# Kernel optimization log

Measured on AMD Instinct MI355X. Metric: run time of the kernel, lower is better.

## Reference

```python
import jax, jax.numpy as jnp
import numpy as np


def setup_inputs() -> dict:
    key = jax.random.key(0)
    k1, k2, k3 = jax.random.split(key, 3)
    B, D, N, C = 4096, 256, 65536, 10
    x = jax.random.normal(k1, (B, D), dtype=jnp.float32)
    keys = jax.random.normal(k2, (N, D), dtype=jnp.float32)
    values = jax.random.uniform(k3, (N, C), dtype=jnp.float32)
    return {"x": x, "keys": keys, "values": values, "k": 8}


def reference(x, keys, values, k):
    # squared euclidean distances [B, N] without materializing diff cube:
    x_sq = jnp.sum(x * x, axis=1, keepdims=True)          # [B,1]
    k_sq = jnp.sum(keys * keys, axis=1)                   # [N]
    dists = x_sq - 2.0 * (x @ keys.T) + k_sq[None, :]     # [B,N]
    neg_top, indices = jax.lax.top_k(-dists, k)           # [B,k]
    hit_values = values[indices]                          # [B,k,C]
    return jnp.sum(hit_values, axis=1) / jnp.float32(k)   # [B,C]
```

## Files before the change

### kernel.cpp

```cpp
#include <hip/hip_runtime.h>
#include <stdint.h>
#include <float.h>

#define B_ROWS 4096
#define N_KEYS 65536
#define DDIM 256
#define NCH 10

#define NSPLIT 8
#define SPLIT_KEYS (N_KEYS / NSPLIT)
#define ROWS_PER_BLK 64
#define CHUNK_KEYS 64
#define NCHUNK (SPLIT_KEYS / CHUNK_KEYS)

typedef float f32x4 __attribute__((ext_vector_type(4)));
typedef short bf16x8 __attribute__((ext_vector_type(8)));

static __device__ __forceinline__ unsigned short f2bf(float f) {
  unsigned u = __float_as_uint(f);
  return (unsigned short)((u + 0x7FFFu + ((u >> 16) & 1u)) >> 16);
}
static __device__ __forceinline__ unsigned ford(float f) {
  unsigned u = __float_as_uint(f);
  return u ^ ((unsigned)((int)u >> 31) | 0x80000000u);
}
static __device__ __forceinline__ unsigned long long shfl_xor_u64(unsigned long long v, int m) {
  unsigned lo = __shfl_xor((unsigned)v, m, 64);
  unsigned hi = __shfl_xor((unsigned)(v >> 32), m, 64);
  return ((unsigned long long)hi << 32) | lo;
}
static __device__ __forceinline__ double shfl_xor_f64(double v, int m) {
  return __longlong_as_double((long long)shfl_xor_u64((unsigned long long)__double_as_longlong(v), m));
}
static __device__ __forceinline__ void gl_lds16(const void* g, void* l) {
  __builtin_amdgcn_global_load_lds(
      (const __attribute__((address_space(1))) unsigned int*)g,
      (__attribute__((address_space(3))) unsigned int*)l, 16, 0, 0);
}

__global__ __launch_bounds__(256) void transpose_keys(const float* __restrict__ keys,
                                                      unsigned char* __restrict__ kbf,
                                                      float* __restrict__ ksq) {
  __shared__ __align__(16) unsigned char T[128 * 512];
  const int t = threadIdx.x;
  const int lane = t & 63;
  const float4* src = (const float4*)(keys + (size_t)blockIdx.x * 128 * DDIM);
#pragma unroll
  for (int j = 0; j < 32; ++j) {
    int g = j * 256 + t;
    float4 v = src[g];
    int key = g >> 6;
    int u = lane >> 1, sub = lane & 1;
    unsigned lo = ((unsigned)f2bf(v.y) << 16) | f2bf(v.x);
    unsigned hi2 = ((unsigned)f2bf(v.w) << 16) | f2bf(v.z);
    unsigned long long p = ((unsigned long long)hi2 << 32) | lo;
    *(unsigned long long*)&T[key * 512 + ((u ^ (key & 7)) << 4) + (sub << 3)] = p;
    float ss = v.x * v.x + v.y * v.y + v.z * v.z + v.w * v.w;
#pragma unroll
    for (int off = 32; off; off >>= 1) ss += __shfl_xor(ss, off, 64);
    if (lane == 0) ksq[blockIdx.x * 128 + key] = ss;
  }
  __syncthreads();
  uint4* dst = (uint4*)(kbf + (size_t)blockIdx.x * 65536);
#pragma unroll
  for (int j = 0; j < 16; ++j) {
    int ou = j * 256 + t;
    int c64 = ou >> 11, rem = ou & 2047;
    int koct = rem >> 6, key64 = rem & 63;
    int keyl = c64 * 64 + key64;
    dst[ou] = *(const uint4*)&T[keyl * 512 + ((koct ^ (keyl & 7)) << 4)];
  }
}

__global__ __launch_bounds__(512, 4) void knn_main(
    const float* __restrict__ x,
    const unsigned char* __restrict__ kbf,
    const float* __restrict__ ksqg,
    unsigned int* __restrict__ pools,
    unsigned int* __restrict__ counts,
    int CAP) {
  __shared__ __align__(16) unsigned char tiles[2][32768];
  __shared__ float tauh[2][2][2][16][4];
  __shared__ unsigned int rowcnt[64];

  const int t = threadIdx.x;
  const int lane = t & 63;
  const int wv = t >> 6;
  const int mw = wv & 3;
  const int ws = wv >> 2;
  const int lo4 = lane & 15;
  const int hi = lane >> 4;

  const int split = blockIdx.x & (NSPLIT - 1);
  const int rb = (blockIdx.x >> 3) * ROWS_PER_BLK;
  const int sb = split * SPLIT_KEYS;

  const int xrow0 = rb + ws * 32 + lo4;
  const int xrow1 = xrow0 + 16;
  const int rl0 = ws * 32 + lo4, rl1 = rl0 + 16;

  bf16x8 xb0[8], xb1[8];
#pragma unroll
  for (int s = 0; s < 8; ++s) {
    const float* p0 = x + (size_t)xrow0 * DDIM + s * 32 + hi * 8;
    const float* p1 = x + (size_t)xrow1 * DDIM + s * 32 + hi * 8;
    float4 a = *(const float4*)p0, b = *(const float4*)(p0 + 4);
    float4 c = *(const float4*)p1, d = *(const float4*)(p1 + 4);
    union { unsigned short us[8]; bf16x8 v; } u0, u1;
    u0.us[0]=f2bf(a.x); u0.us[1]=f2bf(a.y); u0.us[2]=f2bf(a.z); u0.us[3]=f2bf(a.w);
    u0.us[4]=f2bf(b.x); u0.us[5]=f2bf(b.y); u0.us[6]=f2bf(b.z); u0.us[7]=f2bf(b.w);
    u1.us[0]=f2bf(c.x); u1.us[1]=f2bf(c.y); u1.us[2]=f2bf(c.z); u1.us[3]=f2bf(c.w);
    u1.us[4]=f2bf(d.x); u1.us[5]=f2bf(d.y); u1.us[6]=f2bf(d.z); u1.us[7]=f2bf(d.w);
    xb0[s] = u0.v; xb1[s] = u1.v;
  }

  float smin0 = FLT_MAX, smin1 = FLT_MAX;
  const unsigned char* srcbase = kbf + ((size_t)split * NCHUNK << 15);
  const size_t pb0 = ((size_t)xrow0 * NSPLIT + split) * (size_t)CAP;
  const size_t pb1 = ((size_t)xrow1 * NSPLIT + split) * (size_t)CAP;

  auto STAGE = [&](int c, int buf) {
    const unsigned char* src = srcbase + ((size_t)c << 15);
    unsigned char* wb = (unsigned char*)tiles[buf] + ((wv * 64) << 4);
#pragma unroll
    for (int i = 0; i < 4; ++i)
      gl_lds16(src + (((i * 512) + t) << 4), wb + ((i * 512) << 4));
  };

  f32x4 a0, a1;
  float sc0[4], sc1[4];

  auto COMPUTE = [&](int c) {
    const unsigned char* tile = tiles[c & 1];
    a0 = 0.0f; a1 = 0.0f;
#pragma unroll
    for (int s = 0; s < 8; ++s) {
      const unsigned char* rp = tile + (s * 4 + hi) * 1024 + (mw * 16 + lo4) * 16;
      bf16x8 af = *(const bf16x8*)rp;
      a0 = __builtin_amdgcn_mfma_f32_16x16x32_bf16(af, xb0[s], a0, 0, 0, 0);
      a1 = __builtin_amdgcn_mfma_f32_16x16x32_bf16(af, xb1[s], a1, 0, 0, 0);
    }
    float4 kq = *(const float4*)(ksqg + sb + c * CHUNK_KEYS + mw * 16 + hi * 4);
#pragma unroll
    for (int i = 0; i < 4; ++i) {
      sc0[i] = fmaf(-2.0f, a0[i], ((const float*)&kq)[i]);
      sc1[i] = fmaf(-2.0f, a1[i], ((const float*)&kq)[i]);
    }
    float mb0 = fminf(fminf(sc0[0], sc0[1]), fminf(sc0[2], sc0[3]));
    float mb1 = fminf(fminf(sc1[0], sc1[1]), fminf(sc1[2], sc1[3]));
    smin0 = fminf(smin0, mb0);
    smin1 = fminf(smin1, mb1);
  };

  auto PUBLISH = [&](int par) {
    float p0 = fminf(smin0, __shfl_xor(smin0, 16, 64));
    p0 = fmaxf(p0, __shfl_xor(p0, 32, 64));
    float p1 = fminf(smin1, __shfl_xor(smin1, 16, 64));
    p1 = fmaxf(p1, __shfl_xor(p1, 32, 64));
    if (hi == 0) {
      tauh[par][0][ws][lo4][mw] = p0;
      tauh[par][1][ws][lo4][mw] = p1;
    }
  };

  auto APPEND = [&](int c, int par) {
    float4 t0 = *(const float4*)&tauh[par][0][ws][lo4][0];
    float4 t1 = *(const float4*)&tauh[par][1][ws][lo4][0];
    float tau0 = fmaxf(fmaxf(t0.x, t0.y), fmaxf(t0.z, t0.w));
    float tau1 = fmaxf(fmaxf(t1.x, t1.y), fmaxf(t1.z, t1.w));
    int kloc = c * CHUNK_KEYS + mw * 16 + hi * 4;
#pragma unroll
    for (int e = 0; e < 4; ++e) {
      if (sc0[e] <= tau0) {
        unsigned slot = atomicAdd(&rowcnt[rl0], 1u);
        if ((int)slot < CAP)
          pools[pb0 + slot] = (ford(sc0[e]) & 0xFFFFE000u) | (unsigned)(kloc + e);
      }
      if (sc1[e] <= tau1) {
        unsigned slot = atomicAdd(&rowcnt[rl1], 1u);
        if ((int)slot < CAP)
          pools[pb1 + slot] = (ford(sc1[e]) & 0xFFFFE000u) | (unsigned)(kloc + e);
      }
    }
  };

  if (t < 64) rowcnt[t] = 0;
  STAGE(0, 0);
  __syncthreads();
  STAGE(1, 1);
  COMPUTE(0);
  PUBLISH(0);
  PUBLISH(1);
  __syncthreads();
  APPEND(0, 0);

#pragma unroll 1
  for (int c = 1; c < NCHUNK; ++c) {
    const int cn = (c + 1 < NCHUNK) ? c + 1 : c;
    STAGE(cn, (c + 1) & 1);
    COMPUTE(c);
    APPEND(c, (c - 1) & 1);
    PUBLISH(c & 1);
    __syncthreads();
  }

  __syncthreads();
  if (t < 64) counts[(size_t)(rb + t) * NSPLIT + split] = rowcnt[t];
}

__global__ __launch_bounds__(64) void knn_refine(
    const float* __restrict__ x,
    const float* __restrict__ keys,
    const float* __restrict__ ksq,
    const float* __restrict__ values,
    const unsigned int* __restrict__ pools,
    const unsigned int* __restrict__ counts,
    int CAP,
    float* __restrict__ out) {
  __shared__ float4 xl[64];
  const int row = blockIdx.x;
  const int lane = threadIdx.x;

  xl[lane] = ((const float4*)(x + (size_t)row * DDIM))[lane];
  __syncthreads();

  unsigned long long h[8];
#pragma unroll
  for (int i = 0; i < 8; ++i) h[i] = ~0ULL;

  auto insert = [&](unsigned long long v) {
    if (v < h[7]) {
#pragma unroll
      for (int j = 7; j >= 1; --j) {
        unsigned long long a = h[j - 1];
        unsigned long long mx = a > v ? a : v;
        h[j] = (v < h[j]) ? mx : h[j];
      }
      h[0] = h[0] < v ? h[0] : v;
    }
  };

  for (int s = 0; s < NSPLIT; ++s) {
    unsigned cnt = counts[(size_t)row * NSPLIT + s];
    if ((int)cnt <= CAP) {
      const unsigned int* pp = pools + ((size_t)row * NSPLIT + s) * (size_t)CAP;
      for (int i = lane; i < (int)cnt; i += 64) {
        unsigned p = pp[i];
        unsigned long long v = ((unsigned long long)p << 17)
                             | (unsigned)(s * SPLIT_KEYS + (p & 0x1FFFu));
        insert(v);
      }
    } else {
      for (int kk = lane; kk < SPLIT_KEYS; kk += 64) {
        int gk = s * SPLIT_KEYS + kk;
        const float4* kr = (const float4*)(keys + (size_t)gk * DDIM);
        float acc = 0.f;
#pragma unroll 8
        for (int d = 0; d < 64; ++d) {
          float4 kv = kr[d], xv = xl[d];
          acc = fmaf(kv.x, xv.x, acc); acc = fmaf(kv.y, xv.y, acc);
          acc = fmaf(kv.z, xv.z, acc); acc = fmaf(kv.w, xv.w, acc);
        }
        float sc = fmaf(-2.0f, acc, ksq[gk]);
        unsigned p = (ford(sc) & 0xFFFFE000u) | (unsigned)kk;
        insert(((unsigned long long)p << 17) | (unsigned)gk);
      }
    }
  }

  int myidx = 0;
#pragma unroll 1
  for (int r = 0; r < 24; ++r) {
    unsigned long long m = h[0];
#pragma unroll
    for (int off = 32; off; off >>= 1) {
      unsigned long long o = shfl_xor_u64(m, off);
      m = o < m ? o : m;
    }
    if (lane == r) myidx = (int)(m & 0x1FFFFu);
    if (h[0] == m) {
#pragma unroll
      for (int i = 0; i < 7; ++i) h[i] = h[i + 1];
      h[7] = ~0ULL;
    }
  }

  double dv = 1e300;
  if (lane < 24) {
    const float4* kr = (const float4*)(keys + (size_t)myidx * DDIM);
    double s = 0.0;
#pragma unroll 8
    for (int d = 0; d < 64; ++d) {
      float4 kv = kr[d], xv = xl[d];
      double d0 = (double)xv.x - (double)kv.x;
      double d1 = (double)xv.y - (double)kv.y;
      double d2 = (double)xv.z - (double)kv.z;
      double d3 = (double)xv.w - (double)kv.w;
      s += d0 * d0 + d1 * d1 + d2 * d2 + d3 * d3;
    }
    dv = s;
  }

  int di = myidx;
  int chosen[8];
#pragma unroll
  for (int r = 0; r < 8; ++r) {
    double m = dv; int mi = di;
#pragma unroll
    for (int off = 32; off; off >>= 1) {
      double om = shfl_xor_f64(m, off);
      int omi = __shfl_xor(mi, off, 64);
      if (om < m || (om == m && omi < mi)) { m = om; mi = omi; }
    }
    chosen[r] = mi;
    if (di == mi && dv < 1e300) dv = 1e300;
  }

  if (lane < NCH) {
    double a = 0.0;
#pragma unroll
    for (int r = 0; r < 8; ++r) a += (double)values[(size_t)chosen[r] * NCH + lane];
    out[row * NCH + lane] = (float)(a * 0.125);
  }
}

extern "C" void kernel_launch(void* const* d_in, const int* in_sizes, int n_in,
                              void* d_out, int out_size, void* d_ws, size_t ws_size,
                              hipStream_t stream) {
  (void)in_sizes; (void)n_in; (void)out_size;
  const float* x      = (const float*)d_in[0];
  const float* keys   = (const float*)d_in[1];
  const float* values = (const float*)d_in[2];
  float* out = (float*)d_out;

  char* ws = (char*)d_ws;
  unsigned char* kbf = (unsigned char*)ws;
  float* ksq   = (float*)(ws + 33554432);
  unsigned int* counts = (unsigned int*)(ws + 33554432 + 262144);
  unsigned int* pools  = (unsigned int*)(ws + 33554432 + 262144 + 131072);

  size_t base = 33554432 + 262144 + 131072;
  size_t cap = (ws_size > base) ? (ws_size - base) / ((size_t)B_ROWS * NSPLIT * 4) : 32;
  if (cap < 32) cap = 32;
  if (cap > 2048) cap = 2048;
  int CAP = (int)cap;

  transpose_keys<<<N_KEYS / 128, 256, 0, stream>>>(keys, kbf, ksq);
  knn_main<<<(B_ROWS / ROWS_PER_BLK) * NSPLIT, 512, 0, stream>>>(
      x, kbf, ksq, pools, counts, CAP);
  knn_refine<<<B_ROWS, 64, 0, stream>>>(x, keys, ksq, values, pools, counts, CAP, out);
}
```

Baseline: 318.6 us.

## Enlarge row tile per block to reuse staged key tiles across more MFMAs

Each block now processes 256 query rows against a 1/16 key split instead of 64 rows against a 1/8 split. Each wave holds four 16-row x fragments and two key fragments, so every LDS key load feeds more MFMAs and global key traffic per row drops. The threshold selection is reworked so each chunk is filtered against the previous chunk's published per-row thresholds. The loop synchronisation uses explicit waitcnt and barriers with ksq prefetch. Pool index encoding shrinks to 12 bits. Register pressure rises (launch bounds drop to 2 blocks per SIMD) and the grid shrinks to 256 blocks, which may reduce occupancy.

```diff
diff --git a/kernel.cpp b/kernel.cpp
--- a/kernel.cpp
+++ b/kernel.cpp
@@ -7,9 +7,9 @@
 #define DDIM 256
 #define NCH 10
 
-#define NSPLIT 8
+#define NSPLIT 16
 #define SPLIT_KEYS (N_KEYS / NSPLIT)
-#define ROWS_PER_BLK 64
+#define ROWS_PER_BLK 256
 #define CHUNK_KEYS 64
 #define NCHUNK (SPLIT_KEYS / CHUNK_KEYS)
 
@@ -72,7 +72,7 @@
   }
 }
 
-__global__ __launch_bounds__(512, 4) void knn_main(
+__global__ __launch_bounds__(512, 2) void knn_main(
     const float* __restrict__ x,
     const unsigned char* __restrict__ kbf,
     const float* __restrict__ ksqg,
@@ -80,44 +80,39 @@
     unsigned int* __restrict__ counts,
     int CAP) {
   __shared__ __align__(16) unsigned char tiles[2][32768];
-  __shared__ float tauh[2][2][2][16][4];
-  __shared__ unsigned int rowcnt[64];
+  __shared__ float tauh[2][256];
+  __shared__ unsigned int rowcnt[256];
 
   const int t = threadIdx.x;
   const int lane = t & 63;
   const int wv = t >> 6;
-  const int mw = wv & 3;
-  const int ws = wv >> 2;
+  const int kg = wv & 1;
+  const int rq = wv >> 1;
   const int lo4 = lane & 15;
   const int hi = lane >> 4;
 
   const int split = blockIdx.x & (NSPLIT - 1);
-  const int rb = (blockIdx.x >> 3) * ROWS_PER_BLK;
+  const int rb = (blockIdx.x >> 4) * ROWS_PER_BLK;
   const int sb = split * SPLIT_KEYS;
 
-  const int xrow0 = rb + ws * 32 + lo4;
-  const int xrow1 = xrow0 + 16;
-  const int rl0 = ws * 32 + lo4, rl1 = rl0 + 16;
-
-  bf16x8 xb0[8], xb1[8];
-#pragma unroll
-  for (int s = 0; s < 8; ++s) {
-    const float* p0 = x + (size_t)xrow0 * DDIM + s * 32 + hi * 8;
-    const float* p1 = x + (size_t)xrow1 * DDIM + s * 32 + hi * 8;
-    float4 a = *(const float4*)p0, b = *(const float4*)(p0 + 4);
-    float4 c = *(const float4*)p1, d = *(const float4*)(p1 + 4);
-    union { unsigned short us[8]; bf16x8 v; } u0, u1;
-    u0.us[0]=f2bf(a.x); u0.us[1]=f2bf(a.y); u0.us[2]=f2bf(a.z); u0.us[3]=f2bf(a.w);
-    u0.us[4]=f2bf(b.x); u0.us[5]=f2bf(b.y); u0.us[6]=f2bf(b.z); u0.us[7]=f2bf(b.w);
-    u1.us[0]=f2bf(c.x); u1.us[1]=f2bf(c.y); u1.us[2]=f2bf(c.z); u1.us[3]=f2bf(c.w);
-    u1.us[4]=f2bf(d.x); u1.us[5]=f2bf(d.y); u1.us[6]=f2bf(d.z); u1.us[7]=f2bf(d.w);
-    xb0[s] = u0.v; xb1[s] = u1.v;
-  }
-
-  float smin0 = FLT_MAX, smin1 = FLT_MAX;
-  const unsigned char* srcbase = kbf + ((size_t)split * NCHUNK << 15);
-  const size_t pb0 = ((size_t)xrow0 * NSPLIT + split) * (size_t)CAP;
-  const size_t pb1 = ((size_t)xrow1 * NSPLIT + split) * (size_t)CAP;
+  bf16x8 xb[4][8];
+#pragma unroll
+  for (int st = 0; st < 4; ++st) {
+    const float* xr = x + (size_t)(rb + rq * 64 + st * 16 + lo4) * DDIM;
+#pragma unroll
+    for (int s = 0; s < 8; ++s) {
+      const float* p = xr + s * 32 + hi * 8;
+      float4 a = *(const float4*)p, b = *(const float4*)(p + 4);
+      union { unsigned short us[8]; bf16x8 v; } u;
+      u.us[0]=f2bf(a.x); u.us[1]=f2bf(a.y); u.us[2]=f2bf(a.z); u.us[3]=f2bf(a.w);
+      u.us[4]=f2bf(b.x); u.us[5]=f2bf(b.y); u.us[6]=f2bf(b.z); u.us[7]=f2bf(b.w);
+      xb[st][s] = u.v;
+    }
+  }
+
+  if (t < 256) rowcnt[t] = 0;
+
+  const unsigned char* srcbase = kbf + ((size_t)(split * NCHUNK) << 15);
 
   auto STAGE = [&](int c, int buf) {
     const unsigned char* src = srcbase + ((size_t)c << 15);
@@ -127,85 +122,119 @@
       gl_lds16(src + (((i * 512) + t) << 4), wb + ((i * 512) << 4));
   };
 
-  f32x4 a0, a1;
-  float sc0[4], sc1[4];
+  const int kqoff = kg * 32 + hi * 4;
+  float4 kqc0 = *(const float4*)(ksqg + sb + kqoff);
+  float4 kqc1 = *(const float4*)(ksqg + sb + kqoff + 16);
+
+  float smin[4] = {FLT_MAX, FLT_MAX, FLT_MAX, FLT_MAX};
+  f32x4 acc[4][2];
 
   auto COMPUTE = [&](int c) {
     const unsigned char* tile = tiles[c & 1];
-    a0 = 0.0f; a1 = 0.0f;
+#pragma unroll
+    for (int st = 0; st < 4; ++st) { acc[st][0] = 0.0f; acc[st][1] = 0.0f; }
 #pragma unroll
     for (int s = 0; s < 8; ++s) {
-      const unsigned char* rp = tile + (s * 4 + hi) * 1024 + (mw * 16 + lo4) * 16;
-      bf16x8 af = *(const bf16x8*)rp;
-      a0 = __builtin_amdgcn_mfma_f32_16x16x32_bf16(af, xb0[s], a0, 0, 0, 0);
-      a1 = __builtin_amdgcn_mfma_f32_16x16x32_bf16(af, xb1[s], a1, 0, 0, 0);
-    }
-    float4 kq = *(const float4*)(ksqg + sb + c * CHUNK_KEYS + mw * 16 + hi * 4);
-#pragma unroll
-    for (int i = 0; i < 4; ++i) {
-      sc0[i] = fmaf(-2.0f, a0[i], ((const float*)&kq)[i]);
-      sc1[i] = fmaf(-2.0f, a1[i], ((const float*)&kq)[i]);
-    }
-    float mb0 = fminf(fminf(sc0[0], sc0[1]), fminf(sc0[2], sc0[3]));
-    float mb1 = fminf(fminf(sc1[0], sc1[1]), fminf(sc1[2], sc1[3]));
-    smin0 = fminf(smin0, mb0);
-    smin1 = fminf(smin1, mb1);
-  };
-
-  auto PUBLISH = [&](int par) {
-    float p0 = fminf(smin0, __shfl_xor(smin0, 16, 64));
-    p0 = fmaxf(p0, __shfl_xor(p0, 32, 64));
-    float p1 = fminf(smin1, __shfl_xor(smin1, 16, 64));
-    p1 = fmaxf(p1, __shfl_xor(p1, 32, 64));
-    if (hi == 0) {
-      tauh[par][0][ws][lo4][mw] = p0;
-      tauh[par][1][ws][lo4][mw] = p1;
-    }
-  };
-
-  auto APPEND = [&](int c, int par) {
-    float4 t0 = *(const float4*)&tauh[par][0][ws][lo4][0];
-    float4 t1 = *(const float4*)&tauh[par][1][ws][lo4][0];
-    float tau0 = fmaxf(fmaxf(t0.x, t0.y), fmaxf(t0.z, t0.w));
-    float tau1 = fmaxf(fmaxf(t1.x, t1.y), fmaxf(t1.z, t1.w));
-    int kloc = c * CHUNK_KEYS + mw * 16 + hi * 4;
-#pragma unroll
-    for (int e = 0; e < 4; ++e) {
-      if (sc0[e] <= tau0) {
-        unsigned slot = atomicAdd(&rowcnt[rl0], 1u);
-        if ((int)slot < CAP)
-          pools[pb0 + slot] = (ford(sc0[e]) & 0xFFFFE000u) | (unsigned)(kloc + e);
-      }
-      if (sc1[e] <= tau1) {
-        unsigned slot = atomicAdd(&rowcnt[rl1], 1u);
-        if ((int)slot < CAP)
-          pools[pb1 + slot] = (ford(sc1[e]) & 0xFFFFE000u) | (unsigned)(kloc + e);
-      }
-    }
-  };
-
-  if (t < 64) rowcnt[t] = 0;
+      const unsigned char* rp = tile + (s * 4 + hi) * 1024 + (kg * 32 + lo4) * 16;
+      bf16x8 af0 = *(const bf16x8*)rp;
+      bf16x8 af1 = *(const bf16x8*)(rp + 256);
+#pragma unroll
+      for (int st = 0; st < 4; ++st) {
+        acc[st][0] = __builtin_amdgcn_mfma_f32_16x16x32_bf16(af0, xb[st][s], acc[st][0], 0, 0, 0);
+        acc[st][1] = __builtin_amdgcn_mfma_f32_16x16x32_bf16(af1, xb[st][s], acc[st][1], 0, 0, 0);
+      }
+    }
+  };
+
+  auto SELECT = [&](int c, const float* trd) {
+    const int kbase = c * CHUNK_KEYS + kg * 32;
+#pragma unroll
+    for (int st = 0; st < 4; ++st) {
+      float sc[8];
+#pragma unroll
+      for (int i = 0; i < 4; ++i) {
+        sc[i]     = fmaf(-2.0f, acc[st][0][i], ((const float*)&kqc0)[i]);
+        sc[4 + i] = fmaf(-2.0f, acc[st][1][i], ((const float*)&kqc1)[i]);
+      }
+      float m = sc[0];
+#pragma unroll
+      for (int e = 1; e < 8; ++e) m = fminf(m, sc[e]);
+      smin[st] = fminf(smin[st], m);
+      if (m <= trd[st]) {
+        const int lrow = rq * 64 + st * 16 + lo4;
+        const size_t pb = ((size_t)(rb + lrow) * NSPLIT + split) * (size_t)CAP;
+#pragma unroll
+        for (int e = 0; e < 8; ++e) {
+          if (sc[e] <= trd[st]) {
+            unsigned slot = atomicAdd(&rowcnt[lrow], 1u);
+            if ((int)slot < CAP)
+              pools[pb + slot] = (ford(sc[e]) & 0xFFFFF000u)
+                               | (unsigned)(kbase + (e >> 2) * 16 + hi * 4 + (e & 3));
+          }
+        }
+      }
+    }
+  };
+
+  auto PUBLISH = [&]() {
+#pragma unroll
+    for (int st = 0; st < 4; ++st) {
+      float v = smin[st];
+      v = fmaxf(v, __shfl_xor(v, 16, 64));
+      v = fmaxf(v, __shfl_xor(v, 32, 64));
+      if (hi == 0) tauh[kg][rq * 64 + st * 16 + lo4] = v;
+    }
+  };
+
   STAGE(0, 0);
   __syncthreads();
+
   STAGE(1, 1);
+  float4 kqn0 = *(const float4*)(ksqg + sb + 64 + kqoff);
+  float4 kqn1 = *(const float4*)(ksqg + sb + 64 + kqoff + 16);
   COMPUTE(0);
-  PUBLISH(0);
-  PUBLISH(1);
-  __syncthreads();
-  APPEND(0, 0);
+  {
+    float tneg[4] = {-FLT_MAX, -FLT_MAX, -FLT_MAX, -FLT_MAX};
+    SELECT(0, tneg);
+  }
+  PUBLISH();
+  __syncthreads();
+  {
+    float trd[4];
+#pragma unroll
+    for (int st = 0; st < 4; ++st) {
+      int lr = rq * 64 + st * 16 + lo4;
+      trd[st] = fmaxf(tauh[0][lr], tauh[1][lr]);
+    }
+    SELECT(0, trd);
+  }
+  kqc0 = kqn0; kqc1 = kqn1;
 
 #pragma unroll 1
   for (int c = 1; c < NCHUNK; ++c) {
     const int cn = (c + 1 < NCHUNK) ? c + 1 : c;
     STAGE(cn, (c + 1) & 1);
+    float4 kn0 = *(const float4*)(ksqg + sb + cn * 64 + kqoff);
+    float4 kn1 = *(const float4*)(ksqg + sb + cn * 64 + kqoff + 16);
+    float trd[4];
+#pragma unroll
+    for (int st = 0; st < 4; ++st) {
+      int lr = rq * 64 + st * 16 + lo4;
+      trd[st] = fmaxf(tauh[0][lr], tauh[1][lr]);
+    }
+    asm volatile("s_waitcnt vmcnt(6)" ::: "memory");
+    __builtin_amdgcn_s_barrier();
+    __builtin_amdgcn_sched_barrier(0);
     COMPUTE(c);
-    APPEND(c, (c - 1) & 1);
-    PUBLISH(c & 1);
-    __syncthreads();
-  }
-
-  __syncthreads();
-  if (t < 64) counts[(size_t)(rb + t) * NSPLIT + split] = rowcnt[t];
+    SELECT(c, trd);
+    PUBLISH();
+    kqc0 = kn0; kqc1 = kn1;
+    asm volatile("s_waitcnt lgkmcnt(0)" ::: "memory");
+    __builtin_amdgcn_s_barrier();
+  }
+
+  __syncthreads();
+  if (t < 256) counts[(size_t)(rb + t) * NSPLIT + split] = rowcnt[t];
 }
 
 __global__ __launch_bounds__(64) void knn_refine(
@@ -246,8 +275,8 @@
       const unsigned int* pp = pools + ((size_t)row * NSPLIT + s) * (size_t)CAP;
       for (int i = lane; i < (int)cnt; i += 64) {
         unsigned p = pp[i];
-        unsigned long long v = ((unsigned long long)p << 17)
-                             | (unsigned)(s * SPLIT_KEYS + (p & 0x1FFFu));
+        unsigned long long v = ((unsigned long long)p << 16)
+                             | (unsigned)(s * SPLIT_KEYS + (p & 0xFFFu));
         insert(v);
       }
     } else {
@@ -262,8 +291,8 @@
           acc = fmaf(kv.z, xv.z, acc); acc = fmaf(kv.w, xv.w, acc);
         }
         float sc = fmaf(-2.0f, acc, ksq[gk]);
-        unsigned p = (ford(sc) & 0xFFFFE000u) | (unsigned)kk;
-        insert(((unsigned long long)p << 17) | (unsigned)gk);
+        unsigned p = (ford(sc) & 0xFFFFF000u) | (unsigned)kk;
+        insert(((unsigned long long)p << 16) | (unsigned)gk);
       }
     }
   }
@@ -277,7 +306,7 @@
       unsigned long long o = shfl_xor_u64(m, off);
       m = o < m ? o : m;
     }
-    if (lane == r) myidx = (int)(m & 0x1FFFFu);
+    if (lane == r) myidx = (int)(m & 0xFFFFu);
     if (h[0] == m) {
 #pragma unroll
       for (int i = 0; i < 7; ++i) h[i] = h[i + 1];
@@ -337,12 +366,12 @@
   unsigned char* kbf = (unsigned char*)ws;
   float* ksq   = (float*)(ws + 33554432);
   unsigned int* counts = (unsigned int*)(ws + 33554432 + 262144);
-  unsigned int* pools  = (unsigned int*)(ws + 33554432 + 262144 + 131072);
-
-  size_t base = 33554432 + 262144 + 131072;
+  unsigned int* pools  = (unsigned int*)(ws + 33554432 + 262144 + 262144);
+
+  size_t base = 33554432 + 262144 + 262144;
   size_t cap = (ws_size > base) ? (ws_size - base) / ((size_t)B_ROWS * NSPLIT * 4) : 32;
   if (cap < 32) cap = 32;
-  if (cap > 2048) cap = 2048;
+  if (cap > 1024) cap = 1024;
   int CAP = (int)cap;
 
   transpose_keys<<<N_KEYS / 128, 256, 0, stream>>>(keys, kbf, ksq);
```

Result: slower. 341.8 us (+7.3%).

## Restructure kNN main kernel to register-streamed keys with global shared thresholds

Applied to the files above, without the earlier changes.

Replaces the LDS-staged key tiles with direct global-to-register loads of a new key layout. Each wave now holds 64 query rows in registers and streams 16-key slices, with double-buffered prefetch. Splits grow from 8 to 32, and candidates go into one per-row pool through global atomics. A global per-row threshold (atomicMin) is shared across splits to prune appends, and a separate kernel pre-converts x to bf16. The goal is to remove LDS traffic and block-level syncs and to raise MFMA reuse of each key fragment. The cost is more global atomics, heavier register pressure, and some dependence on cross-block threshold timing.

```diff
diff --git a/kernel.cpp b/kernel.cpp
--- a/kernel.cpp
+++ b/kernel.cpp
@@ -7,11 +7,9 @@
 #define DDIM 256
 #define NCH 10
 
-#define NSPLIT 8
+#define NSPLIT 32
 #define SPLIT_KEYS (N_KEYS / NSPLIT)
-#define ROWS_PER_BLK 64
-#define CHUNK_KEYS 64
-#define NCHUNK (SPLIT_KEYS / CHUNK_KEYS)
+#define NSTEP (SPLIT_KEYS / 16)
 
 typedef float f32x4 __attribute__((ext_vector_type(4)));
 typedef short bf16x8 __attribute__((ext_vector_type(8)));
@@ -23,6 +21,10 @@
 static __device__ __forceinline__ unsigned ford(float f) {
   unsigned u = __float_as_uint(f);
   return u ^ ((unsigned)((int)u >> 31) | 0x80000000u);
+}
+static __device__ __forceinline__ float ford_inv(unsigned u) {
+  unsigned m = 0x80000000u | ((u >> 31) - 1u);
+  return __uint_as_float(u ^ m);
 }
 static __device__ __forceinline__ unsigned long long shfl_xor_u64(unsigned long long v, int m) {
   unsigned lo = __shfl_xor((unsigned)v, m, 64);
@@ -31,11 +33,6 @@
 }
 static __device__ __forceinline__ double shfl_xor_f64(double v, int m) {
   return __longlong_as_double((long long)shfl_xor_u64((unsigned long long)__double_as_longlong(v), m));
-}
-static __device__ __forceinline__ void gl_lds16(const void* g, void* l) {
-  __builtin_amdgcn_global_load_lds(
-      (const __attribute__((address_space(1))) unsigned int*)g,
-      (__attribute__((address_space(3))) unsigned int*)l, 16, 0, 0);
 }
 
 __global__ __launch_bounds__(256) void transpose_keys(const float* __restrict__ keys,
@@ -61,151 +58,157 @@
     if (lane == 0) ksq[blockIdx.x * 128 + key] = ss;
   }
   __syncthreads();
-  uint4* dst = (uint4*)(kbf + (size_t)blockIdx.x * 65536);
+  uint4* dstS = (uint4*)(kbf + (size_t)(blockIdx.x >> 4) * ((size_t)SPLIT_KEYS * 512));
+  const int kb0 = (blockIdx.x & 15) * 128;
 #pragma unroll
   for (int j = 0; j < 16; ++j) {
     int ou = j * 256 + t;
-    int c64 = ou >> 11, rem = ou & 2047;
-    int koct = rem >> 6, key64 = rem & 63;
-    int keyl = c64 * 64 + key64;
-    dst[ou] = *(const uint4*)&T[keyl * 512 + ((koct ^ (keyl & 7)) << 4)];
-  }
-}
-
-__global__ __launch_bounds__(512, 4) void knn_main(
-    const float* __restrict__ x,
+    int koct = ou >> 7, keyl = ou & 127;
+    dstS[koct * SPLIT_KEYS + kb0 + keyl] =
+        *(const uint4*)&T[keyl * 512 + ((koct ^ (keyl & 7)) << 4)];
+  }
+}
+
+__global__ __launch_bounds__(256) void xprep(const float* __restrict__ x,
+                                             unsigned char* __restrict__ xbf,
+                                             unsigned int* __restrict__ counts,
+                                             unsigned int* __restrict__ taug) {
+  int u = blockIdx.x * 256 + threadIdx.x;
+  int g = u >> 9, s = (u >> 6) & 7, lane = u & 63;
+  int row = g * 16 + (lane & 15);
+  int d0 = s * 32 + (lane >> 4) * 8;
+  const float* p = x + (size_t)row * DDIM + d0;
+  float4 a = *(const float4*)p, b = *(const float4*)(p + 4);
+  union { unsigned short us[8]; bf16x8 v; } w;
+  w.us[0]=f2bf(a.x); w.us[1]=f2bf(a.y); w.us[2]=f2bf(a.z); w.us[3]=f2bf(a.w);
+  w.us[4]=f2bf(b.x); w.us[5]=f2bf(b.y); w.us[6]=f2bf(b.z); w.us[7]=f2bf(b.w);
+  *(bf16x8*)(xbf + (size_t)u * 16) = w.v;
+  if (u < B_ROWS) { counts[u] = 0; taug[u] = 0xFF7FFFFFu; }
+}
+
+__global__ __launch_bounds__(256, 2) void knn_main(
+    const unsigned char* __restrict__ xbf,
     const unsigned char* __restrict__ kbf,
     const float* __restrict__ ksqg,
-    unsigned int* __restrict__ pools,
+    unsigned long long* __restrict__ pool,
     unsigned int* __restrict__ counts,
+    unsigned int* __restrict__ taug,
     int CAP) {
-  __shared__ __align__(16) unsigned char tiles[2][32768];
-  __shared__ float tauh[2][2][2][16][4];
-  __shared__ unsigned int rowcnt[64];
-
   const int t = threadIdx.x;
   const int lane = t & 63;
   const int wv = t >> 6;
-  const int mw = wv & 3;
-  const int ws = wv >> 2;
   const int lo4 = lane & 15;
   const int hi = lane >> 4;
 
   const int split = blockIdx.x & (NSPLIT - 1);
-  const int rb = (blockIdx.x >> 3) * ROWS_PER_BLK;
+  const int rb = (blockIdx.x >> 5) * 256 + wv * 64;
   const int sb = split * SPLIT_KEYS;
 
-  const int xrow0 = rb + ws * 32 + lo4;
-  const int xrow1 = xrow0 + 16;
-  const int rl0 = ws * 32 + lo4, rl1 = rl0 + 16;
-
-  bf16x8 xb0[8], xb1[8];
-#pragma unroll
-  for (int s = 0; s < 8; ++s) {
-    const float* p0 = x + (size_t)xrow0 * DDIM + s * 32 + hi * 8;
-    const float* p1 = x + (size_t)xrow1 * DDIM + s * 32 + hi * 8;
-    float4 a = *(const float4*)p0, b = *(const float4*)(p0 + 4);
-    float4 c = *(const float4*)p1, d = *(const float4*)(p1 + 4);
-    union { unsigned short us[8]; bf16x8 v; } u0, u1;
-    u0.us[0]=f2bf(a.x); u0.us[1]=f2bf(a.y); u0.us[2]=f2bf(a.z); u0.us[3]=f2bf(a.w);
-    u0.us[4]=f2bf(b.x); u0.us[5]=f2bf(b.y); u0.us[6]=f2bf(b.z); u0.us[7]=f2bf(b.w);
-    u1.us[0]=f2bf(c.x); u1.us[1]=f2bf(c.y); u1.us[2]=f2bf(c.z); u1.us[3]=f2bf(c.w);
-    u1.us[4]=f2bf(d.x); u1.us[5]=f2bf(d.y); u1.us[6]=f2bf(d.z); u1.us[7]=f2bf(d.w);
-    xb0[s] = u0.v; xb1[s] = u1.v;
-  }
-
-  float smin0 = FLT_MAX, smin1 = FLT_MAX;
-  const unsigned char* srcbase = kbf + ((size_t)split * NCHUNK << 15);
-  const size_t pb0 = ((size_t)xrow0 * NSPLIT + split) * (size_t)CAP;
-  const size_t pb1 = ((size_t)xrow1 * NSPLIT + split) * (size_t)CAP;
-
-  auto STAGE = [&](int c, int buf) {
-    const unsigned char* src = srcbase + ((size_t)c << 15);
-    unsigned char* wb = (unsigned char*)tiles[buf] + ((wv * 64) << 4);
-#pragma unroll
-    for (int i = 0; i < 4; ++i)
-      gl_lds16(src + (((i * 512) + t) << 4), wb + ((i * 512) << 4));
-  };
-
-  f32x4 a0, a1;
-  float sc0[4], sc1[4];
-
-  auto COMPUTE = [&](int c) {
-    const unsigned char* tile = tiles[c & 1];
-    a0 = 0.0f; a1 = 0.0f;
-#pragma unroll
-    for (int s = 0; s < 8; ++s) {
-      const unsigned char* rp = tile + (s * 4 + hi) * 1024 + (mw * 16 + lo4) * 16;
-      bf16x8 af = *(const bf16x8*)rp;
-      a0 = __builtin_amdgcn_mfma_f32_16x16x32_bf16(af, xb0[s], a0, 0, 0, 0);
-      a1 = __builtin_amdgcn_mfma_f32_16x16x32_bf16(af, xb1[s], a1, 0, 0, 0);
-    }
-    float4 kq = *(const float4*)(ksqg + sb + c * CHUNK_KEYS + mw * 16 + hi * 4);
-#pragma unroll
-    for (int i = 0; i < 4; ++i) {
-      sc0[i] = fmaf(-2.0f, a0[i], ((const float*)&kq)[i]);
-      sc1[i] = fmaf(-2.0f, a1[i], ((const float*)&kq)[i]);
-    }
-    float mb0 = fminf(fminf(sc0[0], sc0[1]), fminf(sc0[2], sc0[3]));
-    float mb1 = fminf(fminf(sc1[0], sc1[1]), fminf(sc1[2], sc1[3]));
-    smin0 = fminf(smin0, mb0);
-    smin1 = fminf(smin1, mb1);
-  };
-
-  auto PUBLISH = [&](int par) {
-    float p0 = fminf(smin0, __shfl_xor(smin0, 16, 64));
-    p0 = fmaxf(p0, __shfl_xor(p0, 32, 64));
-    float p1 = fminf(smin1, __shfl_xor(smin1, 16, 64));
-    p1 = fmaxf(p1, __shfl_xor(p1, 32, 64));
-    if (hi == 0) {
-      tauh[par][0][ws][lo4][mw] = p0;
-      tauh[par][1][ws][lo4][mw] = p1;
-    }
-  };
-
-  auto APPEND = [&](int c, int par) {
-    float4 t0 = *(const float4*)&tauh[par][0][ws][lo4][0];
-    float4 t1 = *(const float4*)&tauh[par][1][ws][lo4][0];
-    float tau0 = fmaxf(fmaxf(t0.x, t0.y), fmaxf(t0.z, t0.w));
-    float tau1 = fmaxf(fmaxf(t1.x, t1.y), fmaxf(t1.z, t1.w));
-    int kloc = c * CHUNK_KEYS + mw * 16 + hi * 4;
-#pragma unroll
-    for (int e = 0; e < 4; ++e) {
-      if (sc0[e] <= tau0) {
-        unsigned slot = atomicAdd(&rowcnt[rl0], 1u);
-        if ((int)slot < CAP)
-          pools[pb0 + slot] = (ford(sc0[e]) & 0xFFFFE000u) | (unsigned)(kloc + e);
+  bf16x8 xb[4][8];
+#pragma unroll
+  for (int st = 0; st < 4; ++st)
+#pragma unroll
+    for (int s = 0; s < 8; ++s)
+      xb[st][s] = *(const bf16x8*)(xbf +
+          (((size_t)(rb / 16 + st) * 8 + s) * 64 + lane) * 16);
+
+  const unsigned char* kb = kbf + (size_t)split * ((size_t)SPLIT_KEYS * 512)
+                          + hi * ((size_t)SPLIT_KEYS * 16) + lo4 * 16;
+
+  float m1[4][2];
+#pragma unroll
+  for (int st = 0; st < 4; ++st) { m1[st][0] = FLT_MAX; m1[st][1] = FLT_MAX; }
+  float tg[4] = {FLT_MAX, FLT_MAX, FLT_MAX, FLT_MAX};
+
+  bf16x8 afA[8], afB[8];
+  float4 kqA, kqB;
+  f32x4 acc[4];
+
+  auto LOADF = [&](bf16x8* af, int kc) {
+    const unsigned char* p = kb + (size_t)kc * 256;
+#pragma unroll
+    for (int s = 0; s < 8; ++s)
+      af[s] = *(const bf16x8*)(p + (size_t)s * (SPLIT_KEYS * 64));
+  };
+  auto LOADQ = [&](int kc) {
+    return *(const float4*)(ksqg + sb + kc * 16 + hi * 4);
+  };
+  auto MM = [&](bf16x8* af) {
+#pragma unroll
+    for (int st = 0; st < 4; ++st) acc[st] = 0.0f;
+#pragma unroll
+    for (int s = 0; s < 8; ++s)
+#pragma unroll
+      for (int st = 0; st < 4; ++st)
+        acc[st] = __builtin_amdgcn_mfma_f32_16x16x32_bf16(af[s], xb[st][s], acc[st], 0, 0, 0);
+  };
+  auto SEL = [&](float4 kq, int kc, int par, bool append) {
+#pragma unroll
+    for (int st = 0; st < 4; ++st) {
+      float sc[4];
+#pragma unroll
+      for (int i = 0; i < 4; ++i)
+        sc[i] = fmaf(-2.0f, acc[st][i], ((const float*)&kq)[i]);
+      float mn = fminf(fminf(sc[0], sc[1]), fminf(sc[2], sc[3]));
+      m1[st][par] = fminf(m1[st][par], mn);
+      if (append) {
+        float tl = fmaxf(m1[st][0], m1[st][1]);
+        tl = fmaxf(tl, __shfl_xor(tl, 16, 64));
+        tl = fmaxf(tl, __shfl_xor(tl, 32, 64));
+        float tau = fminf(tl, tg[st]);
+        if (mn <= tau) {
+          int row = rb + st * 16 + lo4;
+#pragma unroll
+          for (int i = 0; i < 4; ++i) {
+            if (sc[i] <= tau) {
+              unsigned slot = atomicAdd(&counts[row], 1u);
+              if ((int)slot < CAP)
+                pool[(size_t)row * CAP + slot] =
+                    ((unsigned long long)ford(sc[i]) << 32)
+                  | (unsigned)(sb + kc * 16 + hi * 4 + i);
+            }
+          }
+        }
       }
-      if (sc1[e] <= tau1) {
-        unsigned slot = atomicAdd(&rowcnt[rl1], 1u);
-        if ((int)slot < CAP)
-          pools[pb1 + slot] = (ford(sc1[e]) & 0xFFFFE000u) | (unsigned)(kloc + e);
-      }
-    }
-  };
-
-  if (t < 64) rowcnt[t] = 0;
-  STAGE(0, 0);
-  __syncthreads();
-  STAGE(1, 1);
-  COMPUTE(0);
-  PUBLISH(0);
-  PUBLISH(1);
-  __syncthreads();
-  APPEND(0, 0);
+    }
+  };
+  auto PUBLISH = [&]() {
+#pragma unroll
+    for (int st = 0; st < 4; ++st) {
+      float tl = fmaxf(m1[st][0], m1[st][1]);
+      tl = fmaxf(tl, __shfl_xor(tl, 16, 64));
+      tl = fmaxf(tl, __shfl_xor(tl, 32, 64));
+      int row = rb + st * 16 + lo4;
+      if (hi == 0) atomicMin(&taug[row], ford(tl));
+      tg[st] = fminf(tg[st], ford_inv(taug[row]));
+    }
+  };
 
 #pragma unroll 1
-  for (int c = 1; c < NCHUNK; ++c) {
-    const int cn = (c + 1 < NCHUNK) ? c + 1 : c;
-    STAGE(cn, (c + 1) & 1);
-    COMPUTE(c);
-    APPEND(c, (c - 1) & 1);
-    PUBLISH(c & 1);
-    __syncthreads();
-  }
-
-  __syncthreads();
-  if (t < 64) counts[(size_t)(rb + t) * NSPLIT + split] = rowcnt[t];
+  for (int kc = 0; kc < 8; kc += 2) {
+    LOADF(afA, kc);     kqA = LOADQ(kc);
+    LOADF(afB, kc + 1); kqB = LOADQ(kc + 1);
+    MM(afA); SEL(kqA, kc, 0, false);
+    MM(afB); SEL(kqB, kc + 1, 1, false);
+  }
+  PUBLISH();
+
+  LOADF(afA, 0); kqA = LOADQ(0);
+  LOADF(afB, 1); kqB = LOADQ(1);
+#pragma unroll 1
+  for (int kc = 0; kc < NSTEP; kc += 2) {
+    const int n0 = (kc + 2 < NSTEP) ? kc + 2 : 0;
+    const int n1 = (kc + 3 < NSTEP) ? kc + 3 : 1;
+    MM(afA);
+    LOADF(afA, n0);
+    SEL(kqA, kc, 0, true);
+    kqA = LOADQ(n0);
+    MM(afB);
+    LOADF(afB, n1);
+    SEL(kqB, kc + 1, 1, true);
+    kqB = LOADQ(n1);
+    if ((kc & 7) == 6) PUBLISH();
+  }
 }
 
 __global__ __launch_bounds__(64) void knn_refine(
@@ -213,7 +216,7 @@
     const float* __restrict__ keys,
     const float* __restrict__ ksq,
     const float* __restrict__ values,
-    const unsigned int* __restrict__ pools,
+    const unsigned long long* __restrict__ pool,
     const unsigned int* __restrict__ counts,
     int CAP,
     float* __restrict__ out) {
@@ -227,7 +230,6 @@
   unsigned long long h[8];
 #pragma unroll
   for (int i = 0; i < 8; ++i) h[i] = ~0ULL;
-
   auto insert = [&](unsigned long long v) {
     if (v < h[7]) {
 #pragma unroll
@@ -240,31 +242,22 @@
     }
   };
 
-  for (int s = 0; s < NSPLIT; ++s) {
-    unsigned cnt = counts[(size_t)row * NSPLIT + s];
-    if ((int)cnt <= CAP) {
-      const unsigned int* pp = pools + ((size_t)row * NSPLIT + s) * (size_t)CAP;
-      for (int i = lane; i < (int)cnt; i += 64) {
-        unsigned p = pp[i];
-        unsigned long long v = ((unsigned long long)p << 17)
-                             | (unsigned)(s * SPLIT_KEYS + (p & 0x1FFFu));
-        insert(v);
+  const unsigned cnt = counts[row];
+  if ((int)cnt <= CAP) {
+    const unsigned long long* pp = pool + (size_t)row * CAP;
+    for (int i = lane; i < (int)cnt; i += 64) insert(pp[i]);
+  } else {
+    for (int gk = lane; gk < N_KEYS; gk += 64) {
+      const float4* kr = (const float4*)(keys + (size_t)gk * DDIM);
+      float acc = 0.f;
+#pragma unroll 8
+      for (int d = 0; d < 64; ++d) {
+        float4 kv = kr[d], xv = xl[d];
+        acc = fmaf(kv.x, xv.x, acc); acc = fmaf(kv.y, xv.y, acc);
+        acc = fmaf(kv.z, xv.z, acc); acc = fmaf(kv.w, xv.w, acc);
       }
-    } else {
-      for (int kk = lane; kk < SPLIT_KEYS; kk += 64) {
-        int gk = s * SPLIT_KEYS + kk;
-        const float4* kr = (const float4*)(keys + (size_t)gk * DDIM);
-        float acc = 0.f;
-#pragma unroll 8
-        for (int d = 0; d < 64; ++d) {
-          float4 kv = kr[d], xv = xl[d];
-          acc = fmaf(kv.x, xv.x, acc); acc = fmaf(kv.y, xv.y, acc);
-          acc = fmaf(kv.z, xv.z, acc); acc = fmaf(kv.w, xv.w, acc);
-        }
-        float sc = fmaf(-2.0f, acc, ksq[gk]);
-        unsigned p = (ford(sc) & 0xFFFFE000u) | (unsigned)kk;
-        insert(((unsigned long long)p << 17) | (unsigned)gk);
-      }
+      float sc = fmaf(-2.0f, acc, ksq[gk]);
+      insert(((unsigned long long)ford(sc) << 32) | (unsigned)gk);
     }
   }
 
@@ -277,7 +270,7 @@
       unsigned long long o = shfl_xor_u64(m, off);
       m = o < m ? o : m;
     }
-    if (lane == r) myidx = (int)(m & 0x1FFFFu);
+    if (lane == r) myidx = (int)(m & 0xFFFFu);
     if (h[0] == m) {
 #pragma unroll
       for (int i = 0; i < 7; ++i) h[i] = h[i + 1];
@@ -334,19 +327,23 @@
   float* out = (float*)d_out;
 
   char* ws = (char*)d_ws;
-  unsigned char* kbf = (unsigned char*)ws;
-  float* ksq   = (float*)(ws + 33554432);
-  unsigned int* counts = (unsigned int*)(ws + 33554432 + 262144);
-  unsigned int* pools  = (unsigned int*)(ws + 33554432 + 262144 + 131072);
-
-  size_t base = 33554432 + 262144 + 131072;
-  size_t cap = (ws_size > base) ? (ws_size - base) / ((size_t)B_ROWS * NSPLIT * 4) : 32;
-  if (cap < 32) cap = 32;
+  unsigned char* kbf   = (unsigned char*)ws;
+  unsigned char* xbf   = (unsigned char*)(ws + 33554432);
+  float*         ksq   = (float*)(ws + 33554432 + 2097152);
+  unsigned int*  counts= (unsigned int*)(ws + 33554432 + 2097152 + 262144);
+  unsigned int*  taug  = (unsigned int*)(ws + 33554432 + 2097152 + 262144 + 16384);
+  unsigned long long* pool =
+      (unsigned long long*)(ws + 33554432 + 2097152 + 262144 + 32768);
+
+  size_t base = 33554432 + 2097152 + 262144 + 32768;
+  size_t cap = (ws_size > base) ? (ws_size - base) / ((size_t)B_ROWS * 8) : 256;
+  if (cap < 256) cap = 256;
   if (cap > 2048) cap = 2048;
   int CAP = (int)cap;
 
   transpose_keys<<<N_KEYS / 128, 256, 0, stream>>>(keys, kbf, ksq);
-  knn_main<<<(B_ROWS / ROWS_PER_BLK) * NSPLIT, 512, 0, stream>>>(
-      x, kbf, ksq, pools, counts, CAP);
-  knn_refine<<<B_ROWS, 64, 0, stream>>>(x, keys, ksq, values, pools, counts, CAP, out);
-}
+  xprep<<<512, 256, 0, stream>>>(x, xbf, counts, taug);
+  knn_main<<<(B_ROWS / 256) * NSPLIT, 256, 0, stream>>>(
+      xbf, kbf, ksq, pool, counts, taug, CAP);
+  knn_refine<<<B_ROWS, 64, 0, stream>>>(x, keys, ksq, values, pool, counts, CAP, out);
+}
```

Measured after the change: 919.1 us. 189% more time.

## Fold -2 scaling and key norms into MFMA, rotate chunk order, prefetch norms

Applied to the files above, without the earlier changes.

Pre-scales the query by -2 before the bf16 conversion and seeds the MFMA accumulators with the key squared norms, so the scores come straight out of the matrix multiply with no extra fma pass. The key-norm load is prefetched one chunk ahead, the threshold buffer loses its double buffer and is published only every other chunk, and appends are skipped for lane groups whose minimum already exceeds the threshold. Blocks in different halves of the grid start at different chunk offsets to spread memory traffic, and MFMA sections get raised wave priority. The single-buffered threshold is read and written across one barrier per iteration, which could introduce a race or stale thresholds. Thresholds that are looser or published less often may also admit more pool candidates.

```diff
diff --git a/kernel.cpp b/kernel.cpp
--- a/kernel.cpp
+++ b/kernel.cpp
@@ -80,7 +80,7 @@
     unsigned int* __restrict__ counts,
     int CAP) {
   __shared__ __align__(16) unsigned char tiles[2][32768];
-  __shared__ float tauh[2][2][2][16][4];
+  __shared__ float tauh[2][2][16][4];
   __shared__ unsigned int rowcnt[64];
 
   const int t = threadIdx.x;
@@ -94,6 +94,7 @@
   const int split = blockIdx.x & (NSPLIT - 1);
   const int rb = (blockIdx.x >> 3) * ROWS_PER_BLK;
   const int sb = split * SPLIT_KEYS;
+  const int rot = ((blockIdx.x >> 8) & 1) * (NCHUNK / 2);
 
   const int xrow0 = rb + ws * 32 + lo4;
   const int xrow1 = xrow0 + 16;
@@ -107,32 +108,42 @@
     float4 a = *(const float4*)p0, b = *(const float4*)(p0 + 4);
     float4 c = *(const float4*)p1, d = *(const float4*)(p1 + 4);
     union { unsigned short us[8]; bf16x8 v; } u0, u1;
-    u0.us[0]=f2bf(a.x); u0.us[1]=f2bf(a.y); u0.us[2]=f2bf(a.z); u0.us[3]=f2bf(a.w);
-    u0.us[4]=f2bf(b.x); u0.us[5]=f2bf(b.y); u0.us[6]=f2bf(b.z); u0.us[7]=f2bf(b.w);
-    u1.us[0]=f2bf(c.x); u1.us[1]=f2bf(c.y); u1.us[2]=f2bf(c.z); u1.us[3]=f2bf(c.w);
-    u1.us[4]=f2bf(d.x); u1.us[5]=f2bf(d.y); u1.us[6]=f2bf(d.z); u1.us[7]=f2bf(d.w);
+    u0.us[0]=f2bf(-2.f*a.x); u0.us[1]=f2bf(-2.f*a.y); u0.us[2]=f2bf(-2.f*a.z); u0.us[3]=f2bf(-2.f*a.w);
+    u0.us[4]=f2bf(-2.f*b.x); u0.us[5]=f2bf(-2.f*b.y); u0.us[6]=f2bf(-2.f*b.z); u0.us[7]=f2bf(-2.f*b.w);
+    u1.us[0]=f2bf(-2.f*c.x); u1.us[1]=f2bf(-2.f*c.y); u1.us[2]=f2bf(-2.f*c.z); u1.us[3]=f2bf(-2.f*c.w);
+    u1.us[4]=f2bf(-2.f*d.x); u1.us[5]=f2bf(-2.f*d.y); u1.us[6]=f2bf(-2.f*d.z); u1.us[7]=f2bf(-2.f*d.w);
     xb0[s] = u0.v; xb1[s] = u1.v;
   }
 
+  if (t < 64) rowcnt[t] = 0;
+
   float smin0 = FLT_MAX, smin1 = FLT_MAX;
-  const unsigned char* srcbase = kbf + ((size_t)split * NCHUNK << 15);
+  const unsigned char* srcbase = kbf + ((size_t)(split * NCHUNK) << 15);
   const size_t pb0 = ((size_t)xrow0 * NSPLIT + split) * (size_t)CAP;
   const size_t pb1 = ((size_t)xrow1 * NSPLIT + split) * (size_t)CAP;
 
+  auto CIDX = [&](int c) { return (c + rot) & (NCHUNK - 1); };
+
   auto STAGE = [&](int c, int buf) {
-    const unsigned char* src = srcbase + ((size_t)c << 15);
+    const unsigned char* src = srcbase + ((size_t)CIDX(c) << 15);
     unsigned char* wb = (unsigned char*)tiles[buf] + ((wv * 64) << 4);
 #pragma unroll
     for (int i = 0; i < 4; ++i)
       gl_lds16(src + (((i * 512) + t) << 4), wb + ((i * 512) << 4));
   };
+  auto LOADQ = [&](int c) {
+    return *(const float4*)(ksqg + sb + CIDX(c) * CHUNK_KEYS + mw * 16 + hi * 4);
+  };
 
   f32x4 a0, a1;
-  float sc0[4], sc1[4];
+  float4 kqc, kqn;
 
   auto COMPUTE = [&](int c) {
     const unsigned char* tile = tiles[c & 1];
-    a0 = 0.0f; a1 = 0.0f;
+    f32x4 ini;
+    ini[0] = kqc.x; ini[1] = kqc.y; ini[2] = kqc.z; ini[3] = kqc.w;
+    a0 = ini; a1 = ini;
+    __builtin_amdgcn_s_setprio(1);
 #pragma unroll
     for (int s = 0; s < 8; ++s) {
       const unsigned char* rp = tile + (s * 4 + hi) * 1024 + (mw * 16 + lo4) * 16;
@@ -140,67 +151,84 @@
       a0 = __builtin_amdgcn_mfma_f32_16x16x32_bf16(af, xb0[s], a0, 0, 0, 0);
       a1 = __builtin_amdgcn_mfma_f32_16x16x32_bf16(af, xb1[s], a1, 0, 0, 0);
     }
-    float4 kq = *(const float4*)(ksqg + sb + c * CHUNK_KEYS + mw * 16 + hi * 4);
-#pragma unroll
-    for (int i = 0; i < 4; ++i) {
-      sc0[i] = fmaf(-2.0f, a0[i], ((const float*)&kq)[i]);
-      sc1[i] = fmaf(-2.0f, a1[i], ((const float*)&kq)[i]);
-    }
-    float mb0 = fminf(fminf(sc0[0], sc0[1]), fminf(sc0[2], sc0[3]));
-    float mb1 = fminf(fminf(sc1[0], sc1[1]), fminf(sc1[2], sc1[3]));
+    __builtin_amdgcn_s_setprio(0);
+  };
+
+  auto SEL = [&](int c, bool append, float tau0, float tau1) {
+    float mb0 = fminf(fminf(a0[0], a0[1]), fminf(a0[2], a0[3]));
+    float mb1 = fminf(fminf(a1[0], a1[1]), fminf(a1[2], a1[3]));
     smin0 = fminf(smin0, mb0);
     smin1 = fminf(smin1, mb1);
-  };
-
-  auto PUBLISH = [&](int par) {
+    if (append) {
+      const int kloc = CIDX(c) * CHUNK_KEYS + mw * 16 + hi * 4;
+      if (mb0 <= tau0) {
+#pragma unroll
+        for (int i = 0; i < 4; ++i) {
+          if (a0[i] <= tau0) {
+            unsigned slot = atomicAdd(&rowcnt[rl0], 1u);
+            if ((int)slot < CAP)
+              pools[pb0 + slot] = (ford(a0[i]) & 0xFFFFE000u) | (unsigned)(kloc + i);
+          }
+        }
+      }
+      if (mb1 <= tau1) {
+#pragma unroll
+        for (int i = 0; i < 4; ++i) {
+          if (a1[i] <= tau1) {
+            unsigned slot = atomicAdd(&rowcnt[rl1], 1u);
+            if ((int)slot < CAP)
+              pools[pb1 + slot] = (ford(a1[i]) & 0xFFFFE000u) | (unsigned)(kloc + i);
+          }
+        }
+      }
+    }
+  };
+
+  auto RDTAU = [&](float& tau0, float& tau1) {
+    float4 t0 = *(const float4*)&tauh[0][ws][lo4][0];
+    float4 t1 = *(const float4*)&tauh[1][ws][lo4][0];
+    tau0 = fmaxf(fmaxf(t0.x, t0.y), fmaxf(t0.z, t0.w));
+    tau1 = fmaxf(fmaxf(t1.x, t1.y), fmaxf(t1.z, t1.w));
+  };
+
+  auto PUBLISH = [&]() {
     float p0 = fminf(smin0, __shfl_xor(smin0, 16, 64));
     p0 = fmaxf(p0, __shfl_xor(p0, 32, 64));
     float p1 = fminf(smin1, __shfl_xor(smin1, 16, 64));
     p1 = fmaxf(p1, __shfl_xor(p1, 32, 64));
     if (hi == 0) {
-      tauh[par][0][ws][lo4][mw] = p0;
-      tauh[par][1][ws][lo4][mw] = p1;
-    }
-  };
-
-  auto APPEND = [&](int c, int par) {
-    float4 t0 = *(const float4*)&tauh[par][0][ws][lo4][0];
-    float4 t1 = *(const float4*)&tauh[par][1][ws][lo4][0];
-    float tau0 = fmaxf(fmaxf(t0.x, t0.y), fmaxf(t0.z, t0.w));
-    float tau1 = fmaxf(fmaxf(t1.x, t1.y), fmaxf(t1.z, t1.w));
-    int kloc = c * CHUNK_KEYS + mw * 16 + hi * 4;
-#pragma unroll
-    for (int e = 0; e < 4; ++e) {
-      if (sc0[e] <= tau0) {
-        unsigned slot = atomicAdd(&rowcnt[rl0], 1u);
-        if ((int)slot < CAP)
-          pools[pb0 + slot] = (ford(sc0[e]) & 0xFFFFE000u) | (unsigned)(kloc + e);
-      }
-      if (sc1[e] <= tau1) {
-        unsigned slot = atomicAdd(&rowcnt[rl1], 1u);
-        if ((int)slot < CAP)
-          pools[pb1 + slot] = (ford(sc1[e]) & 0xFFFFE000u) | (unsigned)(kloc + e);
-      }
-    }
-  };
-
-  if (t < 64) rowcnt[t] = 0;
+      tauh[0][ws][lo4][mw] = p0;
+      tauh[1][ws][lo4][mw] = p1;
+    }
+  };
+
   STAGE(0, 0);
+  kqc = LOADQ(0);
   __syncthreads();
   STAGE(1, 1);
+  kqn = LOADQ(1);
   COMPUTE(0);
-  PUBLISH(0);
-  PUBLISH(1);
-  __syncthreads();
-  APPEND(0, 0);
+  SEL(0, false, 0.f, 0.f);
+  PUBLISH();
+  __syncthreads();
+  {
+    float tau0, tau1;
+    RDTAU(tau0, tau1);
+    SEL(0, true, tau0, tau1);
+  }
+  kqc = kqn;
 
 #pragma unroll 1
   for (int c = 1; c < NCHUNK; ++c) {
     const int cn = (c + 1 < NCHUNK) ? c + 1 : c;
     STAGE(cn, (c + 1) & 1);
+    kqn = LOADQ(cn);
+    float tau0, tau1;
+    RDTAU(tau0, tau1);
     COMPUTE(c);
-    APPEND(c, (c - 1) & 1);
-    PUBLISH(c & 1);
+    SEL(c, true, tau0, tau1);
+    if (c & 1) PUBLISH();
+    kqc = kqn;
     __syncthreads();
   }
 
```

After: 301.3 us. 5.4% less time.
